# Optimization experiments

Measured on AMD Instinct MI355X. Metric: run time of the kernel, lower is better.

The kernel has to match this reference:

```python
import jax, jax.numpy as jnp
import numpy as np

N_NODES = 100000
N_EDGES = 800000
N_GRAPHS = 500
IN_FEATS = 64
NUM_CLASSES = 4


def setup_inputs() -> dict:
    key = jax.random.key(0)
    ks = jax.random.split(key, 12)

    def glorot(k, shape):
        lim = float(np.sqrt(6.0 / (shape[0] + shape[1])))
        return jax.random.uniform(k, shape, jnp.float32, -lim, lim)

    x = jax.random.normal(ks[0], (N_NODES, IN_FEATS), jnp.float32)
    src = jax.random.randint(ks[1], (N_EDGES,), 0, N_NODES, jnp.int32)
    dst = jax.random.randint(ks[2], (N_EDGES,), 0, N_NODES, jnp.int32)
    graph_ids = jnp.sort(jax.random.randint(ks[3], (N_NODES,), 0, N_GRAPHS, jnp.int32))
    return {
        "x": x,
        "W1": glorot(ks[4], (IN_FEATS, 128)), "b1": jnp.zeros((128,), jnp.float32),
        "W2": glorot(ks[5], (128, 64)),       "b2": jnp.zeros((64,), jnp.float32),
        "W3": glorot(ks[6], (64, 32)),        "b3": jnp.zeros((32,), jnp.float32),
        "W4": glorot(ks[7], (32, NUM_CLASSES)), "b4": jnp.zeros((NUM_CLASSES,), jnp.float32),
        "src": src, "dst": dst, "graph_ids": graph_ids,
    }


def _graph_conv(h, W, b, src, dst, norm_out, norm_in):
    # DGL GraphConv, norm='both': h' = D_in^{-1/2} A D_out^{-1/2} h W + b
    # Apply W first when it reduces feature width (same math, less traffic).
    if h.shape[-1] > W.shape[-1]:
        h = h @ W
        msg = (h * norm_out[:, None])[src]            # [E, d_out]
        agg = jax.ops.segment_sum(msg, dst, num_segments=h.shape[0])
        return agg * norm_in[:, None] + b
    msg = (h * norm_out[:, None])[src]                # [E, d_in]
    agg = jax.ops.segment_sum(msg, dst, num_segments=h.shape[0])
    return (agg * norm_in[:, None]) @ W + b


def reference(x, W1, b1, W2, b2, W3, b3, W4, b4, src, dst, graph_ids):
    n = x.shape[0]
    ones_e = jnp.ones(src.shape, jnp.float32)
    deg_out = jax.ops.segment_sum(ones_e, src, num_segments=n)
    deg_in = jax.ops.segment_sum(ones_e, dst, num_segments=n)
    norm_out = jax.lax.rsqrt(jnp.maximum(deg_out, 1.0))
    norm_in = jax.lax.rsqrt(jnp.maximum(deg_in, 1.0))

    h = jax.nn.relu(_graph_conv(x, W1, b1, src, dst, norm_out, norm_in))
    h = jax.nn.relu(_graph_conv(h, W2, b2, src, dst, norm_out, norm_in))
    h = jax.nn.relu(_graph_conv(h, W3, b3, src, dst, norm_out, norm_in))
    h = _graph_conv(h, W4, b4, src, dst, norm_out, norm_in)

    # dgl.mean_nodes: per-graph mean of node features
    sums = jax.ops.segment_sum(h, graph_ids, num_segments=N_GRAPHS)
    counts = jax.ops.segment_sum(jnp.ones((n,), jnp.float32), graph_ids, num_segments=N_GRAPHS)
    return sums / jnp.maximum(counts, 1.0)[:, None]
```

## Files before the change

### kernel.cpp

```cpp
#include <hip/hip_runtime.h>
#include <hip/hip_bf16.h>


#define TILE 4096
#define SLOT 8192

__global__ __launch_bounds__(256) void k_buildbins(
        const int* __restrict__ src, const int* __restrict__ dst, int E, int NBIN,
        int* __restrict__ cntD, int* __restrict__ cntS,
        int* __restrict__ bucketD, unsigned short* __restrict__ bucketS) {
    __shared__ int ssrc[TILE];
    __shared__ int sdst[TILE];
    __shared__ int hD[256], hS[256], bD[256], bS[256];
    int t = threadIdx.x;
    hD[t] = 0; hS[t] = 0;
    __syncthreads();
    int base = blockIdx.x * TILE;
    int lim = min(TILE, E - base);
#pragma unroll
    for (int k = 0; k < TILE / 256; k++) {
        int i = k * 256 + t;
        if (i < lim) {
            int d = dst[base + i], sv = src[base + i];
            sdst[i] = d; ssrc[i] = sv;
            atomicAdd(&hD[d >> 9], 1);
            atomicAdd(&hS[sv >> 9], 1);
        }
    }
    __syncthreads();
    if (t < NBIN) {
        bD[t] = (hD[t] > 0) ? atomicAdd(&cntD[t], hD[t]) : 0;
        bS[t] = (hS[t] > 0) ? atomicAdd(&cntS[t], hS[t]) : 0;
        hD[t] = 0; hS[t] = 0;
    }
    __syncthreads();
#pragma unroll
    for (int k = 0; k < TILE / 256; k++) {
        int i = k * 256 + t;
        if (i < lim) {
            int d = sdst[i], sv = ssrc[i];
            int binD = d >> 9, binS = sv >> 9;
            int pD = atomicAdd(&hD[binD], 1) + bD[binD];
            bucketD[binD * SLOT + pD] = (sv << 9) | (d & 511);
            int pS = atomicAdd(&hS[binS], 1) + bS[binS];
            bucketS[binS * SLOT + pS] = (unsigned short)(sv & 511);
        }
    }
}

__global__ __launch_bounds__(256) void k_degout(const unsigned short* __restrict__ bucketS,
                                                const int* __restrict__ cntS,
                                                int N, float* __restrict__ norm_out) {
    __shared__ int cnt[512];
    int t = threadIdx.x;
    cnt[t] = 0; cnt[t + 256] = 0;
    __syncthreads();
    int bin = blockIdx.x;
    int b0 = bin * SLOT, cn = cntS[bin];
    for (int j = t; j < cn; j += 256) atomicAdd(&cnt[bucketS[b0 + j]], 1);
    __syncthreads();
    int base = bin << 9;
    for (int l = t; l < 512; l += 256) {
        int g = base + l;
        if (g < N) norm_out[g] = rsqrtf(fmaxf((float)cnt[l], 1.0f));
    }
}

__global__ __launch_bounds__(256) void k_build(const int* __restrict__ bucketD,
                                               const int* __restrict__ cntDg,
                                               const float* __restrict__ norm_out,
                                               int N, int2* __restrict__ rowBE,
                                               float* __restrict__ norm_in,
                                               int2* __restrict__ edges) {
    __shared__ int cnt[512], sc[512];
    int t = threadIdx.x;
    cnt[t] = 0; cnt[t + 256] = 0;
    __syncthreads();
    int bin = blockIdx.x;
    int b0 = bin * SLOT, cn = cntDg[bin];
    for (int j = t; j < cn; j += 256) atomicAdd(&cnt[bucketD[b0 + j] & 511], 1);
    __syncthreads();
    sc[t] = cnt[t]; sc[t + 256] = cnt[t + 256];
    __syncthreads();
    for (int off = 1; off < 512; off <<= 1) {
        int v0 = (t >= off) ? sc[t - off] : 0;
        int i1 = t + 256;
        int v1 = sc[i1 - off];
        __syncthreads();
        sc[t] += v0; sc[i1] += v1;
        __syncthreads();
    }
    int base = bin << 9;
    for (int l = t; l < 512; l += 256) {
        int g = base + l;
        int e = sc[l] - cnt[l];
        if (g < N) {
            rowBE[g] = make_int2(b0 + e, b0 + sc[l]);
            norm_in[g] = rsqrtf(fmaxf((float)cnt[l], 1.0f));
        }
        cnt[l] = e;
    }
    __syncthreads();
    for (int j = t; j < cn; j += 256) {
        int p = bucketD[b0 + j];
        int sv = p >> 9, dl = p & 511;
        int pos = atomicAdd(&cnt[dl], 1);
        edges[b0 + pos] = make_int2(sv, __float_as_int(norm_out[sv]));
    }
}

template <int G>
__device__ __forceinline__ float4 gather_row(const float4* __restrict__ h4,
                                             const int2* __restrict__ edges,
                                             int j, int end, int lane) {
    float4 acc = make_float4(0.f, 0.f, 0.f, 0.f);
    for (; j + 7 < end; j += 8) {
        int2 e[8];
        float4 v[8];
#pragma unroll
        for (int q = 0; q < 8; q++) e[q] = edges[j + q];
#pragma unroll
        for (int q = 0; q < 8; q++) v[q] = h4[(size_t)e[q].x * G + lane];
#pragma unroll
        for (int q = 0; q < 8; q++) {
            float wq = __int_as_float(e[q].y);
            acc.x += v[q].x * wq; acc.y += v[q].y * wq;
            acc.z += v[q].z * wq; acc.w += v[q].w * wq;
        }
    }
    if (j + 3 < end) {
        int2 e0 = edges[j], e1 = edges[j + 1], e2 = edges[j + 2], e3 = edges[j + 3];
        float4 v0 = h4[(size_t)e0.x * G + lane];
        float4 v1 = h4[(size_t)e1.x * G + lane];
        float4 v2 = h4[(size_t)e2.x * G + lane];
        float4 v3 = h4[(size_t)e3.x * G + lane];
        float w0 = __int_as_float(e0.y), w1 = __int_as_float(e1.y);
        float w2 = __int_as_float(e2.y), w3 = __int_as_float(e3.y);
        acc.x += v0.x * w0 + v1.x * w1 + v2.x * w2 + v3.x * w3;
        acc.y += v0.y * w0 + v1.y * w1 + v2.y * w2 + v3.y * w3;
        acc.z += v0.z * w0 + v1.z * w1 + v2.z * w2 + v3.z * w3;
        acc.w += v0.w * w0 + v1.w * w1 + v2.w * w2 + v3.w * w3;
        j += 4;
    }
    for (; j < end; j++) {
        int2 e = edges[j];
        float4 v = h4[(size_t)e.x * G + lane];
        float w0 = __int_as_float(e.y);
        acc.x += v.x * w0; acc.y += v.y * w0; acc.z += v.z * w0; acc.w += v.w * w0;
    }
    return acc;
}

__global__ __launch_bounds__(256) void k_fused1(const float4* __restrict__ x4,
                        const int2* __restrict__ edges, const int2* __restrict__ rowBE,
                        const float* __restrict__ norm, const float* __restrict__ W1,
                        const float* __restrict__ b1, const float* __restrict__ W2,
                        int N, float* __restrict__ t2) {
    constexpr int AP = 33;
    __shared__ float4 Alds[32 * AP];
    __shared__ float  Wlds[2048];
    int t = threadIdx.x;
    int row0 = blockIdx.x * 32;
#pragma unroll
    for (int pass = 0; pass < 2; pass++) {
        int r = pass * 16 + (t >> 4);
        int lane = t & 15;
        int node = row0 + r;
        float4 acc = make_float4(0.f, 0.f, 0.f, 0.f);
        if (node < N) {
            int2 be = rowBE[node];
            acc = gather_row<16>(x4, edges, be.x, be.y, lane);
            float s = norm[node];
            acc.x *= s; acc.y *= s; acc.z *= s; acc.w *= s;
        }
        Alds[lane * AP + r] = acc;
    }
    int tx = t & 31, ty = t >> 5;
    float acc1[4][4] = {};
#pragma unroll 1
    for (int c = 0; c < 4; c++) {
        ((float4*)Wlds)[t]       = ((const float4*)(W1 + c * 16 * 128))[t];
        ((float4*)Wlds)[t + 256] = ((const float4*)(W1 + c * 16 * 128))[t + 256];
        __syncthreads();
#pragma unroll
        for (int k4l = 0; k4l < 4; k4l++) {
            int k4 = c * 4 + k4l;
            float4 a0 = Alds[k4 * AP + ty * 4 + 0];
            float4 a1 = Alds[k4 * AP + ty * 4 + 1];
            float4 a2 = Alds[k4 * AP + ty * 4 + 2];
            float4 a3 = Alds[k4 * AP + ty * 4 + 3];
            const float* wb = &Wlds[(k4l * 4) * 128 + tx * 4];
            float4 w0 = *(const float4*)(wb);
            float4 w1 = *(const float4*)(wb + 128);
            float4 w2 = *(const float4*)(wb + 256);
            float4 w3 = *(const float4*)(wb + 384);
#define GSTEP(AK, WV) \
            acc1[0][0] += a0.AK * WV.x; acc1[0][1] += a0.AK * WV.y; acc1[0][2] += a0.AK * WV.z; acc1[0][3] += a0.AK * WV.w; \
            acc1[1][0] += a1.AK * WV.x; acc1[1][1] += a1.AK * WV.y; acc1[1][2] += a1.AK * WV.z; acc1[1][3] += a1.AK * WV.w; \
            acc1[2][0] += a2.AK * WV.x; acc1[2][1] += a2.AK * WV.y; acc1[2][2] += a2.AK * WV.z; acc1[2][3] += a2.AK * WV.w; \
            acc1[3][0] += a3.AK * WV.x; acc1[3][1] += a3.AK * WV.y; acc1[3][2] += a3.AK * WV.z; acc1[3][3] += a3.AK * WV.w;
            GSTEP(x, w0) GSTEP(y, w1) GSTEP(z, w2) GSTEP(w, w3)
        }
        __syncthreads();
    }
    float4 bb = *(const float4*)(b1 + tx * 4);
    float4 h[4];
#pragma unroll
    for (int i = 0; i < 4; i++) {
        h[i].x = fmaxf(acc1[i][0] + bb.x, 0.f);
        h[i].y = fmaxf(acc1[i][1] + bb.y, 0.f);
        h[i].z = fmaxf(acc1[i][2] + bb.z, 0.f);
        h[i].w = fmaxf(acc1[i][3] + bb.w, 0.f);
    }
#pragma unroll
    for (int i = 0; i < 4; i++) Alds[tx * AP + ty * 4 + i] = h[i];
    int tx2 = t & 15, ty2 = t >> 4;
    float acc2[2][4] = {};
#pragma unroll 1
    for (int c = 0; c < 4; c++) {
        ((float4*)Wlds)[t]       = ((const float4*)(W2 + c * 32 * 64))[t];
        ((float4*)Wlds)[t + 256] = ((const float4*)(W2 + c * 32 * 64))[t + 256];
        __syncthreads();
#pragma unroll
        for (int k4l = 0; k4l < 8; k4l++) {
            int k4 = c * 8 + k4l;
            float4 a0 = Alds[k4 * AP + ty2 * 2 + 0];
            float4 a1 = Alds[k4 * AP + ty2 * 2 + 1];
            const float* wb = &Wlds[(k4l * 4) * 64 + tx2 * 4];
            float4 w0 = *(const float4*)(wb);
            float4 w1 = *(const float4*)(wb + 64);
            float4 w2 = *(const float4*)(wb + 128);
            float4 w3 = *(const float4*)(wb + 192);
#define GSTEP2(AK, WV) \
            acc2[0][0] += a0.AK * WV.x; acc2[0][1] += a0.AK * WV.y; acc2[0][2] += a0.AK * WV.z; acc2[0][3] += a0.AK * WV.w; \
            acc2[1][0] += a1.AK * WV.x; acc2[1][1] += a1.AK * WV.y; acc2[1][2] += a1.AK * WV.z; acc2[1][3] += a1.AK * WV.w;
            GSTEP2(x, w0) GSTEP2(y, w1) GSTEP2(z, w2) GSTEP2(w, w3)
#undef GSTEP2
        }
        __syncthreads();
    }
#pragma unroll
    for (int i = 0; i < 2; i++) {
        int grow = row0 + ty2 * 2 + i;
        if (grow < N) {
            float4 o = make_float4(acc2[i][0], acc2[i][1], acc2[i][2], acc2[i][3]);
            *(float4*)(t2 + (size_t)grow * 64 + tx2 * 4) = o;
        }
    }
#undef GSTEP
}

__global__ __launch_bounds__(256) void k_fused2(const float4* __restrict__ t2_4,
                        const int2* __restrict__ edges, const int2* __restrict__ rowBE,
                        const float* __restrict__ norm, const float* __restrict__ b2,
                        const float* __restrict__ W3, int N, float* __restrict__ t3) {
    constexpr int AP = 33;
    __shared__ float4 Alds[16 * AP];
    __shared__ float  Wlds[64 * 32];
    int t = threadIdx.x;
    int row0 = blockIdx.x * 32;
#pragma unroll
    for (int pass = 0; pass < 2; pass++) {
        int r = pass * 16 + (t >> 4);
        int lane = t & 15;
        int node = row0 + r;
        float4 acc = make_float4(0.f, 0.f, 0.f, 0.f);
        if (node < N) {
            int2 be = rowBE[node];
            acc = gather_row<16>(t2_4, edges, be.x, be.y, lane);
            float s = norm[node];
            float4 b = ((const float4*)b2)[lane];
            acc.x = fmaxf(acc.x * s + b.x, 0.f);
            acc.y = fmaxf(acc.y * s + b.y, 0.f);
            acc.z = fmaxf(acc.z * s + b.z, 0.f);
            acc.w = fmaxf(acc.w * s + b.w, 0.f);
        }
        Alds[lane * AP + r] = acc;
    }
    for (int idx = t; idx < 64 * 32 / 4; idx += 256)
        ((float4*)Wlds)[idx] = ((const float4*)W3)[idx];
    __syncthreads();
    int tx = t & 7, ty = t >> 3;
    float acc3[4] = {};
#pragma unroll 2
    for (int k4 = 0; k4 < 16; k4++) {
        float4 a = Alds[k4 * AP + ty];
        const float* wb = &Wlds[(k4 * 4) * 32 + tx * 4];
        float4 w0 = *(const float4*)(wb);
        float4 w1 = *(const float4*)(wb + 32);
        float4 w2 = *(const float4*)(wb + 64);
        float4 w3 = *(const float4*)(wb + 96);
        acc3[0] += a.x * w0.x + a.y * w1.x + a.z * w2.x + a.w * w3.x;
        acc3[1] += a.x * w0.y + a.y * w1.y + a.z * w2.y + a.w * w3.y;
        acc3[2] += a.x * w0.z + a.y * w1.z + a.z * w2.z + a.w * w3.z;
        acc3[3] += a.x * w0.w + a.y * w1.w + a.z * w2.w + a.w * w3.w;
    }
    int grow = row0 + ty;
    if (grow < N) {
        float4 o = make_float4(acc3[0], acc3[1], acc3[2], acc3[3]);
        *(float4*)(t3 + (size_t)grow * 32 + tx * 4) = o;
    }
}

__global__ __launch_bounds__(256) void k_aggw4(const float4* __restrict__ h4,
                        const int2* __restrict__ edges, const int2* __restrict__ rowBE,
                        const float* __restrict__ norm, const float4* __restrict__ b3_4,
                        const float* __restrict__ W4, int n, float4* __restrict__ t4) {
    __shared__ float w[128];
    if (threadIdx.x < 128) w[threadIdx.x] = W4[threadIdx.x];
    __syncthreads();
    int node = blockIdx.x * 32 + threadIdx.x / 8;
    int lane = threadIdx.x % 8;
    if (node >= n) return;
    float4 wr0 = ((const float4*)w)[4 * lane + 0];
    float4 wr1 = ((const float4*)w)[4 * lane + 1];
    float4 wr2 = ((const float4*)w)[4 * lane + 2];
    float4 wr3 = ((const float4*)w)[4 * lane + 3];
    int2 be = rowBE[node];
    float4 acc = gather_row<8>(h4, edges, be.x, be.y, lane);
    float s = norm[node];
    float4 b = b3_4[lane];
    float hx = fmaxf(acc.x * s + b.x, 0.f);
    float hy = fmaxf(acc.y * s + b.y, 0.f);
    float hz = fmaxf(acc.z * s + b.z, 0.f);
    float hw = fmaxf(acc.w * s + b.w, 0.f);
    float4 p;
    p.x = hx * wr0.x + hy * wr1.x + hz * wr2.x + hw * wr3.x;
    p.y = hx * wr0.y + hy * wr1.y + hz * wr2.y + hw * wr3.y;
    p.z = hx * wr0.z + hy * wr1.z + hz * wr2.z + hw * wr3.z;
    p.w = hx * wr0.w + hy * wr1.w + hz * wr2.w + hw * wr3.w;
#pragma unroll
    for (int m = 1; m < 8; m <<= 1) {
        p.x += __shfl_xor(p.x, m);
        p.y += __shfl_xor(p.y, m);
        p.z += __shfl_xor(p.z, m);
        p.w += __shfl_xor(p.w, m);
    }
    if (lane == 0) t4[node] = p;
}

__global__ __launch_bounds__(256) void k_aggpool(const float4* __restrict__ t4,
                        const int2* __restrict__ edges, const int2* __restrict__ rowBE,
                        const float* __restrict__ norm, const float* __restrict__ b4,
                        const int* __restrict__ gid, int N,
                        float* __restrict__ sums, float* __restrict__ counts) {
    int n = blockIdx.x * blockDim.x + threadIdx.x;
    int lane = threadIdx.x & 63;
    bool valid = (n < N);
    float v0 = 0.f, v1 = 0.f, v2 = 0.f, v3 = 0.f, cnt = 0.f;
    int g = -1;
    if (valid) {
        g = gid[n];
        int2 be = rowBE[n];
        float4 acc = gather_row<1>(t4, edges, be.x, be.y, 0);
        float s = norm[n];
        v0 = acc.x * s + b4[0];
        v1 = acc.y * s + b4[1];
        v2 = acc.z * s + b4[2];
        v3 = acc.w * s + b4[3];
        cnt = 1.f;
    }
#pragma unroll
    for (int off = 1; off < 64; off <<= 1) {
        float u0 = __shfl_up(v0, off);
        float u1 = __shfl_up(v1, off);
        float u2 = __shfl_up(v2, off);
        float u3 = __shfl_up(v3, off);
        float uc = __shfl_up(cnt, off);
        int   ug = __shfl_up(g, off);
        if (lane >= off && ug == g) { v0 += u0; v1 += u1; v2 += u2; v3 += u3; cnt += uc; }
    }
    int gnext = __shfl_down(g, 1);
    bool boundary = (lane == 63) || (gnext != g);
    if (boundary && valid) {
        atomicAdd(&sums[g * 4 + 0], v0);
        atomicAdd(&sums[g * 4 + 1], v1);
        atomicAdd(&sums[g * 4 + 2], v2);
        atomicAdd(&sums[g * 4 + 3], v3);
        atomicAdd(&counts[g], cnt);
    }
}

__global__ void k_div(const float* __restrict__ sums, const float* __restrict__ counts,
                      int G, float* __restrict__ out) {
    int idx = blockIdx.x * blockDim.x + threadIdx.x;
    if (idx >= G * 4) return;
    out[idx] = sums[idx] / fmaxf(counts[idx >> 2], 1.0f);
}

extern "C" void kernel_launch(void* const* d_in, const int* in_sizes, int n_in,
                              void* d_out, int out_size, void* d_ws, size_t ws_size,
                              hipStream_t stream) {
    const float* x  = (const float*)d_in[0];
    const float* W1 = (const float*)d_in[1];
    const float* b1 = (const float*)d_in[2];
    const float* W2 = (const float*)d_in[3];
    const float* b2 = (const float*)d_in[4];
    const float* W3 = (const float*)d_in[5];
    const float* b3 = (const float*)d_in[6];
    const float* W4 = (const float*)d_in[7];
    const float* b4 = (const float*)d_in[8];
    const int* src = (const int*)d_in[9];
    const int* dst = (const int*)d_in[10];
    const int* gid = (const int*)d_in[11];

    const int N = in_sizes[0] / 64;
    const int E = in_sizes[9];
    const int G = out_size / 4;
    const int NP = ((N + 63) / 64) * 64;
    const int NBIN = (N + 511) >> 9;
    const int T = (E + TILE - 1) / TILE;

    char* ws = (char*)d_ws;
    size_t off = 0;
    auto alloc = [&](size_t bytes) -> void* {
        void* p = (void*)(ws + off);
        off += (bytes + 255) & ~(size_t)255;
        return p;
    };
    float* sums     = (float*)alloc(2048 * 4);
    float* counts   = (float*)alloc(512 * 4);
    int*   cntD     = (int*)alloc(256 * 4);
    int*   cntS     = (int*)alloc(256 * 4);
    int*   bucketD  = (int*)alloc((size_t)NBIN * SLOT * 4);
    unsigned short* bucketS = (unsigned short*)alloc((size_t)NBIN * SLOT * 2);
    int2*  edges    = (int2*)alloc((size_t)NBIN * SLOT * 8);
    int2*  rowBE    = (int2*)alloc((size_t)NP * 8);
    float* norm_out = (float*)alloc((size_t)NP * 4);
    float* norm_in  = (float*)alloc((size_t)NP * 4);
    float* t2buf    = (float*)alloc((size_t)N * 64 * 4);
    float* t3buf    = (float*)alloc((size_t)N * 32 * 4);
    float* t4buf    = (float*)alloc((size_t)N * 4 * 4);

    hipMemsetAsync(sums, 0, (2048 + 512 + 256 + 256) * 4, stream);

    k_buildbins<<<T, 256, 0, stream>>>(src, dst, E, NBIN, cntD, cntS, bucketD, bucketS);
    k_degout<<<NBIN, 256, 0, stream>>>(bucketS, cntS, N, norm_out);
    k_build<<<NBIN, 256, 0, stream>>>(bucketD, cntD, norm_out, N, rowBE, norm_in, edges);

    int fb = (N + 31) / 32;
    int nb = (N + 255) / 256;
    k_fused1<<<fb, 256, 0, stream>>>((const float4*)x, edges, rowBE, norm_in,
                                     W1, b1, W2, N, t2buf);
    k_fused2<<<fb, 256, 0, stream>>>((const float4*)t2buf, edges, rowBE, norm_in,
                                     b2, W3, N, t3buf);
    k_aggw4<<<fb, 256, 0, stream>>>((const float4*)t3buf, edges, rowBE,
                                    norm_in, (const float4*)b3, W4, N,
                                    (float4*)t4buf);
    k_aggpool<<<nb, 256, 0, stream>>>((const float4*)t4buf, edges, rowBE,
                                      norm_in, b4, gid, N, sums, counts);
    k_div<<<(G * 4 + 255) / 256, 256, 0, stream>>>(sums, counts, G, (float*)d_out);
}
```

Measured before the change: 194.3 us.

## Process 64 rows per block in fused GCN layers with register-prefetched weights

The two fused gather+GEMM kernels now handle 64 nodes per block instead of 32. Each thread computes more output rows (8x4 and 4x4 for the first kernel, 2x4 for the second), so every weight value read from shared memory is reused across more rows. Weight chunks are now 256 float4 and are prefetched into a register one step ahead of the shared-memory store, which overlaps the global load with compute. The first kernel gets a launch_bounds occupancy hint of 4, and the padded LDS layout widens to 65. The cost is higher register pressure and half as many blocks, which could reduce latency hiding in the gather phase.

Result: slower. 209.2 us (+7.7%).

```diff
diff --git a/kernel.cpp b/kernel.cpp
--- a/kernel.cpp
+++ b/kernel.cpp
@@ -151,18 +151,21 @@
     return acc;
 }
 
-__global__ __launch_bounds__(256) void k_fused1(const float4* __restrict__ x4,
+__global__ __launch_bounds__(256, 4) void k_fused1(const float4* __restrict__ x4,
                         const int2* __restrict__ edges, const int2* __restrict__ rowBE,
                         const float* __restrict__ norm, const float* __restrict__ W1,
                         const float* __restrict__ b1, const float* __restrict__ W2,
                         int N, float* __restrict__ t2) {
-    constexpr int AP = 33;
+    constexpr int AP = 65;
     __shared__ float4 Alds[32 * AP];
-    __shared__ float  Wlds[2048];
+    __shared__ float  Wlds[1024];
     int t = threadIdx.x;
-    int row0 = blockIdx.x * 32;
-#pragma unroll
-    for (int pass = 0; pass < 2; pass++) {
+    int row0 = blockIdx.x * 64;
+    const float4* W1v = (const float4*)W1;
+    const float4* W2v = (const float4*)W2;
+    float4 wreg = W1v[t];
+#pragma unroll
+    for (int pass = 0; pass < 4; pass++) {
         int r = pass * 16 + (t >> 4);
         int lane = t & 15;
         int node = row0 + r;
@@ -176,91 +179,94 @@
         Alds[lane * AP + r] = acc;
     }
     int tx = t & 31, ty = t >> 5;
-    float acc1[4][4] = {};
+    float acc1[8][4] = {};
 #pragma unroll 1
-    for (int c = 0; c < 4; c++) {
-        ((float4*)Wlds)[t]       = ((const float4*)(W1 + c * 16 * 128))[t];
-        ((float4*)Wlds)[t + 256] = ((const float4*)(W1 + c * 16 * 128))[t + 256];
-        __syncthreads();
-#pragma unroll
-        for (int k4l = 0; k4l < 4; k4l++) {
-            int k4 = c * 4 + k4l;
-            float4 a0 = Alds[k4 * AP + ty * 4 + 0];
-            float4 a1 = Alds[k4 * AP + ty * 4 + 1];
-            float4 a2 = Alds[k4 * AP + ty * 4 + 2];
-            float4 a3 = Alds[k4 * AP + ty * 4 + 3];
+    for (int c = 0; c < 8; c++) {
+        __syncthreads();
+        ((float4*)Wlds)[t] = wreg;
+        __syncthreads();
+        if (c < 7) wreg = W1v[(c + 1) * 256 + t];
+#pragma unroll
+        for (int k4l = 0; k4l < 2; k4l++) {
+            int k4 = c * 2 + k4l;
+            const float4* ab = &Alds[k4 * AP + ty * 8];
             const float* wb = &Wlds[(k4l * 4) * 128 + tx * 4];
             float4 w0 = *(const float4*)(wb);
             float4 w1 = *(const float4*)(wb + 128);
             float4 w2 = *(const float4*)(wb + 256);
             float4 w3 = *(const float4*)(wb + 384);
-#define GSTEP(AK, WV) \
-            acc1[0][0] += a0.AK * WV.x; acc1[0][1] += a0.AK * WV.y; acc1[0][2] += a0.AK * WV.z; acc1[0][3] += a0.AK * WV.w; \
-            acc1[1][0] += a1.AK * WV.x; acc1[1][1] += a1.AK * WV.y; acc1[1][2] += a1.AK * WV.z; acc1[1][3] += a1.AK * WV.w; \
-            acc1[2][0] += a2.AK * WV.x; acc1[2][1] += a2.AK * WV.y; acc1[2][2] += a2.AK * WV.z; acc1[2][3] += a2.AK * WV.w; \
-            acc1[3][0] += a3.AK * WV.x; acc1[3][1] += a3.AK * WV.y; acc1[3][2] += a3.AK * WV.z; acc1[3][3] += a3.AK * WV.w;
-            GSTEP(x, w0) GSTEP(y, w1) GSTEP(z, w2) GSTEP(w, w3)
-        }
-        __syncthreads();
-    }
+#pragma unroll
+            for (int i = 0; i < 8; i++) {
+                float4 a = ab[i];
+                acc1[i][0] += a.x * w0.x + a.y * w1.x + a.z * w2.x + a.w * w3.x;
+                acc1[i][1] += a.x * w0.y + a.y * w1.y + a.z * w2.y + a.w * w3.y;
+                acc1[i][2] += a.x * w0.z + a.y * w1.z + a.z * w2.z + a.w * w3.z;
+                acc1[i][3] += a.x * w0.w + a.y * w1.w + a.z * w2.w + a.w * w3.w;
+            }
+        }
+    }
+    __syncthreads();
     float4 bb = *(const float4*)(b1 + tx * 4);
-    float4 h[4];
-#pragma unroll
-    for (int i = 0; i < 4; i++) {
-        h[i].x = fmaxf(acc1[i][0] + bb.x, 0.f);
-        h[i].y = fmaxf(acc1[i][1] + bb.y, 0.f);
-        h[i].z = fmaxf(acc1[i][2] + bb.z, 0.f);
-        h[i].w = fmaxf(acc1[i][3] + bb.w, 0.f);
-    }
-#pragma unroll
-    for (int i = 0; i < 4; i++) Alds[tx * AP + ty * 4 + i] = h[i];
+    wreg = W2v[t];
+#pragma unroll
+    for (int i = 0; i < 8; i++) {
+        float4 h;
+        h.x = fmaxf(acc1[i][0] + bb.x, 0.f);
+        h.y = fmaxf(acc1[i][1] + bb.y, 0.f);
+        h.z = fmaxf(acc1[i][2] + bb.z, 0.f);
+        h.w = fmaxf(acc1[i][3] + bb.w, 0.f);
+        Alds[tx * AP + ty * 8 + i] = h;
+    }
     int tx2 = t & 15, ty2 = t >> 4;
-    float acc2[2][4] = {};
+    float acc2[4][4] = {};
 #pragma unroll 1
-    for (int c = 0; c < 4; c++) {
-        ((float4*)Wlds)[t]       = ((const float4*)(W2 + c * 32 * 64))[t];
-        ((float4*)Wlds)[t + 256] = ((const float4*)(W2 + c * 32 * 64))[t + 256];
-        __syncthreads();
-#pragma unroll
-        for (int k4l = 0; k4l < 8; k4l++) {
-            int k4 = c * 8 + k4l;
-            float4 a0 = Alds[k4 * AP + ty2 * 2 + 0];
-            float4 a1 = Alds[k4 * AP + ty2 * 2 + 1];
+    for (int c = 0; c < 8; c++) {
+        __syncthreads();
+        ((float4*)Wlds)[t] = wreg;
+        __syncthreads();
+        if (c < 7) wreg = W2v[(c + 1) * 256 + t];
+#pragma unroll
+        for (int k4l = 0; k4l < 4; k4l++) {
+            int k4 = c * 4 + k4l;
+            const float4* ab = &Alds[k4 * AP + ty2 * 4];
             const float* wb = &Wlds[(k4l * 4) * 64 + tx2 * 4];
             float4 w0 = *(const float4*)(wb);
             float4 w1 = *(const float4*)(wb + 64);
             float4 w2 = *(const float4*)(wb + 128);
             float4 w3 = *(const float4*)(wb + 192);
-#define GSTEP2(AK, WV) \
-            acc2[0][0] += a0.AK * WV.x; acc2[0][1] += a0.AK * WV.y; acc2[0][2] += a0.AK * WV.z; acc2[0][3] += a0.AK * WV.w; \
-            acc2[1][0] += a1.AK * WV.x; acc2[1][1] += a1.AK * WV.y; acc2[1][2] += a1.AK * WV.z; acc2[1][3] += a1.AK * WV.w;
-            GSTEP2(x, w0) GSTEP2(y, w1) GSTEP2(z, w2) GSTEP2(w, w3)
-#undef GSTEP2
-        }
-        __syncthreads();
-    }
-#pragma unroll
-    for (int i = 0; i < 2; i++) {
-        int grow = row0 + ty2 * 2 + i;
+#pragma unroll
+            for (int i = 0; i < 4; i++) {
+                float4 a = ab[i];
+                acc2[i][0] += a.x * w0.x + a.y * w1.x + a.z * w2.x + a.w * w3.x;
+                acc2[i][1] += a.x * w0.y + a.y * w1.y + a.z * w2.y + a.w * w3.y;
+                acc2[i][2] += a.x * w0.z + a.y * w1.z + a.z * w2.z + a.w * w3.z;
+                acc2[i][3] += a.x * w0.w + a.y * w1.w + a.z * w2.w + a.w * w3.w;
+            }
+        }
+    }
+#pragma unroll
+    for (int i = 0; i < 4; i++) {
+        int grow = row0 + ty2 * 4 + i;
         if (grow < N) {
             float4 o = make_float4(acc2[i][0], acc2[i][1], acc2[i][2], acc2[i][3]);
             *(float4*)(t2 + (size_t)grow * 64 + tx2 * 4) = o;
         }
     }
-#undef GSTEP
 }
 
 __global__ __launch_bounds__(256) void k_fused2(const float4* __restrict__ t2_4,
                         const int2* __restrict__ edges, const int2* __restrict__ rowBE,
                         const float* __restrict__ norm, const float* __restrict__ b2,
                         const float* __restrict__ W3, int N, float* __restrict__ t3) {
-    constexpr int AP = 33;
+    constexpr int AP = 65;
     __shared__ float4 Alds[16 * AP];
     __shared__ float  Wlds[64 * 32];
     int t = threadIdx.x;
-    int row0 = blockIdx.x * 32;
-#pragma unroll
-    for (int pass = 0; pass < 2; pass++) {
+    int row0 = blockIdx.x * 64;
+    float4 wr0 = ((const float4*)W3)[t];
+    float4 wr1 = ((const float4*)W3)[t + 256];
+#pragma unroll
+    for (int pass = 0; pass < 4; pass++) {
         int r = pass * 16 + (t >> 4);
         int lane = t & 15;
         int node = row0 + r;
@@ -277,28 +283,36 @@
         }
         Alds[lane * AP + r] = acc;
     }
-    for (int idx = t; idx < 64 * 32 / 4; idx += 256)
-        ((float4*)Wlds)[idx] = ((const float4*)W3)[idx];
+    ((float4*)Wlds)[t] = wr0;
+    ((float4*)Wlds)[t + 256] = wr1;
     __syncthreads();
     int tx = t & 7, ty = t >> 3;
-    float acc3[4] = {};
+    float acc3[2][4] = {};
 #pragma unroll 2
     for (int k4 = 0; k4 < 16; k4++) {
-        float4 a = Alds[k4 * AP + ty];
+        float4 a0 = Alds[k4 * AP + ty * 2 + 0];
+        float4 a1 = Alds[k4 * AP + ty * 2 + 1];
         const float* wb = &Wlds[(k4 * 4) * 32 + tx * 4];
         float4 w0 = *(const float4*)(wb);
         float4 w1 = *(const float4*)(wb + 32);
         float4 w2 = *(const float4*)(wb + 64);
         float4 w3 = *(const float4*)(wb + 96);
-        acc3[0] += a.x * w0.x + a.y * w1.x + a.z * w2.x + a.w * w3.x;
-        acc3[1] += a.x * w0.y + a.y * w1.y + a.z * w2.y + a.w * w3.y;
-        acc3[2] += a.x * w0.z + a.y * w1.z + a.z * w2.z + a.w * w3.z;
-        acc3[3] += a.x * w0.w + a.y * w1.w + a.z * w2.w + a.w * w3.w;
-    }
-    int grow = row0 + ty;
-    if (grow < N) {
-        float4 o = make_float4(acc3[0], acc3[1], acc3[2], acc3[3]);
-        *(float4*)(t3 + (size_t)grow * 32 + tx * 4) = o;
+        acc3[0][0] += a0.x * w0.x + a0.y * w1.x + a0.z * w2.x + a0.w * w3.x;
+        acc3[0][1] += a0.x * w0.y + a0.y * w1.y + a0.z * w2.y + a0.w * w3.y;
+        acc3[0][2] += a0.x * w0.z + a0.y * w1.z + a0.z * w2.z + a0.w * w3.z;
+        acc3[0][3] += a0.x * w0.w + a0.y * w1.w + a0.z * w2.w + a0.w * w3.w;
+        acc3[1][0] += a1.x * w0.x + a1.y * w1.x + a1.z * w2.x + a1.w * w3.x;
+        acc3[1][1] += a1.x * w0.y + a1.y * w1.y + a1.z * w2.y + a1.w * w3.y;
+        acc3[1][2] += a1.x * w0.z + a1.y * w1.z + a1.z * w2.z + a1.w * w3.z;
+        acc3[1][3] += a1.x * w0.w + a1.y * w1.w + a1.z * w2.w + a1.w * w3.w;
+    }
+#pragma unroll
+    for (int i = 0; i < 2; i++) {
+        int grow = row0 + ty * 2 + i;
+        if (grow < N) {
+            float4 o = make_float4(acc3[i][0], acc3[i][1], acc3[i][2], acc3[i][3]);
+            *(float4*)(t3 + (size_t)grow * 32 + tx * 4) = o;
+        }
     }
 }
 
@@ -438,15 +452,16 @@
     k_degout<<<NBIN, 256, 0, stream>>>(bucketS, cntS, N, norm_out);
     k_build<<<NBIN, 256, 0, stream>>>(bucketD, cntD, norm_out, N, rowBE, norm_in, edges);
 
-    int fb = (N + 31) / 32;
+    int fb64 = (N + 63) / 64;
+    int fb32 = (N + 31) / 32;
     int nb = (N + 255) / 256;
-    k_fused1<<<fb, 256, 0, stream>>>((const float4*)x, edges, rowBE, norm_in,
-                                     W1, b1, W2, N, t2buf);
-    k_fused2<<<fb, 256, 0, stream>>>((const float4*)t2buf, edges, rowBE, norm_in,
-                                     b2, W3, N, t3buf);
-    k_aggw4<<<fb, 256, 0, stream>>>((const float4*)t3buf, edges, rowBE,
-                                    norm_in, (const float4*)b3, W4, N,
-                                    (float4*)t4buf);
+    k_fused1<<<fb64, 256, 0, stream>>>((const float4*)x, edges, rowBE, norm_in,
+                                       W1, b1, W2, N, t2buf);
+    k_fused2<<<fb64, 256, 0, stream>>>((const float4*)t2buf, edges, rowBE, norm_in,
+                                       b2, W3, N, t3buf);
+    k_aggw4<<<fb32, 256, 0, stream>>>((const float4*)t3buf, edges, rowBE,
+                                      norm_in, (const float4*)b3, W4, N,
+                                      (float4*)t4buf);
     k_aggpool<<<nb, 256, 0, stream>>>((const float4*)t4buf, edges, rowBE,
                                       norm_in, b4, gid, N, sums, counts);
     k_div<<<(G * 4 + 255) / 256, 256, 0, stream>>>(sums, counts, G, (float*)d_out);
```
